# Optimization experiments

Hardware: AMD Instinct MI355X
Metric: run time of the kernel (lower is better)

The kernel has to match this reference:

```python
import jax, jax.numpy as jnp
import numpy as np

B, LT, D, N, H = 16, 512, 1024, 4096, 16
LN_EPS = 1e-5


def setup_inputs() -> dict:
    key = jax.random.key(0)
    ks = jax.random.split(key, 10)
    s = 0.02
    struct_token = jax.random.normal(ks[0], (N, D), dtype=jnp.float32)
    text_token = jax.random.normal(ks[1], (B, LT, D), dtype=jnp.float32)
    # contiguous, sorted segment ids: 256 struct tokens per batch element
    struct_batch = jnp.repeat(jnp.arange(B, dtype=jnp.int32), N // B)
    return {
        "struct_token": struct_token,
        "text_token": text_token,
        "in_proj_w": jax.random.normal(ks[2], (3 * D, D), dtype=jnp.float32) * s,
        "in_proj_b": jnp.zeros((3 * D,), jnp.float32),
        "attn_out_w": jax.random.normal(ks[3], (D, D), dtype=jnp.float32) * s,
        "attn_out_b": jnp.zeros((D,), jnp.float32),
        "ln_g": jnp.ones((D,), jnp.float32),
        "ln_b": jnp.zeros((D,), jnp.float32),
        "proj_w": jax.random.normal(ks[4], (D, D), dtype=jnp.float32) * s,
        "proj_b": jnp.zeros((D,), jnp.float32),
        "struct_batch": struct_batch,
        "L_max": N // B,
    }


def reference(struct_token, text_token, in_proj_w, in_proj_b, attn_out_w,
              attn_out_b, ln_g, ln_b, proj_w, proj_b, struct_batch, L_max):
    Bq = text_token.shape[0]
    Dm = struct_token.shape[-1]
    dh = Dm // H
    Ntok = struct_token.shape[0]

    # ---- ragged pad-pack (struct_batch is sorted/contiguous per segment) ----
    counts = jnp.bincount(struct_batch, length=Bq)                 # [B]
    starts = jnp.concatenate([jnp.zeros((1,), counts.dtype),
                              jnp.cumsum(counts)[:-1]])            # [B]
    pos = jnp.arange(Ntok) - starts[struct_batch]                  # [N] position in segment
    padded = jnp.zeros((Bq, L_max, Dm), struct_token.dtype)
    padded = padded.at[struct_batch, pos].set(struct_token)        # [B, Ls, D]

    # ---- nn.MultiheadAttention (batch_first): Q=padded, K=V=text ----
    wq, wk, wv = in_proj_w[:Dm], in_proj_w[Dm:2 * Dm], in_proj_w[2 * Dm:]
    bq, bk, bv = in_proj_b[:Dm], in_proj_b[Dm:2 * Dm], in_proj_b[2 * Dm:]
    q = (padded @ wq.T + bq).reshape(Bq, L_max, H, dh)
    k = (text_token @ wk.T + bk).reshape(Bq, -1, H, dh)
    v = (text_token @ wv.T + bv).reshape(Bq, -1, H, dh)
    scores = jnp.einsum('bqhd,bkhd->bhqk', q, k) / jnp.sqrt(jnp.float32(dh))
    attn = jax.nn.softmax(scores, axis=-1)
    ctx = jnp.einsum('bhqk,bkhd->bqhd', attn, v).reshape(Bq, L_max, Dm)
    fused = ctx @ attn_out_w.T + attn_out_b                        # [B, Ls, D]

    # ---- LayerNorm + output projection ----
    mu = fused.mean(-1, keepdims=True)
    var = fused.var(-1, keepdims=True)
    fused = (fused - mu) * jax.lax.rsqrt(var + LN_EPS) * ln_g + ln_b
    fused = fused @ proj_w.T + proj_b

    # ---- unpack valid tokens + scatter-mean over segments ----
    tok = fused[struct_batch, pos]                                 # [N, D]
    seg_sum = jax.ops.segment_sum(tok, struct_batch, num_segments=Bq)
    return seg_sum / jnp.maximum(counts, 1)[:, None].astype(seg_sum.dtype)
```

## Files before the change

kernel.cpp:

```cpp
#include <hip/hip_runtime.h>

constexpr int B  = 16;
constexpr int LT = 512;
constexpr int D  = 1024;
constexpr int N  = 4096;
constexpr int H  = 16;
constexpr int DH = D / H;
constexpr int LMAX = N / B;
constexpr float LN_EPS = 1e-5f;

typedef short  s16x8 __attribute__((ext_vector_type(8)));
typedef float  f32x4 __attribute__((ext_vector_type(4)));

__device__ __forceinline__ unsigned short f2bf(float x) {
    unsigned int u = __float_as_uint(x);
    unsigned int r = (u + 0x7fffu + ((u >> 16) & 1u)) >> 16;
    return (unsigned short)r;
}

__device__ __forceinline__ void load_lds16(const void* g, void* l) {
    __builtin_amdgcn_global_load_lds(
        (const __attribute__((address_space(1))) unsigned int*)g,
        (__attribute__((address_space(3))) unsigned int*)l, 16, 0, 0);
}

__global__ void prep_kernel(const int* __restrict__ sb, int* __restrict__ counts,
                            int* __restrict__ starts, int* __restrict__ pos) {
    __shared__ int s_counts[B], s_starts[B];
    int t = threadIdx.x;
    if (t < B) s_counts[t] = 0;
    __syncthreads();
    for (int i = t; i < N; i += 256) atomicAdd(&s_counts[sb[i]], 1);
    __syncthreads();
    if (t == 0) {
        int run = 0;
        for (int b = 0; b < B; b++) { s_starts[b] = run; run += s_counts[b]; }
    }
    __syncthreads();
    if (t < B) { counts[t] = s_counts[t]; starts[t] = s_starts[t]; }
    for (int i = t; i < N; i += 256) {
        int b = sb[i];
        pos[i] = i - s_starts[b];
    }
}

__global__ void scatter_kernel(const float* __restrict__ st, const int* __restrict__ sb,
                               const int* __restrict__ pos, unsigned short* __restrict__ padded) {
    int i = blockIdx.x;
    int b = sb[i], p = pos[i];
    int d = threadIdx.x * 4;
    float4 v = *(const float4*)&st[(size_t)i * D + d];
    ushort4 o;
    o.x = f2bf(v.x); o.y = f2bf(v.y); o.z = f2bf(v.z); o.w = f2bf(v.w);
    *(ushort4*)&padded[((size_t)(b * LMAX + p)) * D + d] = o;
}

__global__ __launch_bounds__(256) void cast3_kernel(
        const float* __restrict__ x0, unsigned short* __restrict__ y0, int n0,
        const float* __restrict__ x1, unsigned short* __restrict__ y1, int n1,
        const float* __restrict__ x2, unsigned short* __restrict__ y2, int n2) {
    long long i = (long long)(blockIdx.x * 256 + threadIdx.x) * 8;
    const float* x; unsigned short* y;
    if (i < n0)                { x = x0 + i; y = y0 + i; }
    else if (i < (long long)n0 + n1) { long long j = i - n0; x = x1 + j; y = y1 + j; }
    else if (i < (long long)n0 + n1 + n2) { long long j = i - n0 - n1; x = x2 + j; y = y2 + j; }
    else return;
    float4 a = *(const float4*)x;
    float4 b = *(const float4*)(x + 4);
    ushort4 o1, o2;
    o1.x = f2bf(a.x); o1.y = f2bf(a.y); o1.z = f2bf(a.z); o1.w = f2bf(a.w);
    o2.x = f2bf(b.x); o2.y = f2bf(b.y); o2.z = f2bf(b.z); o2.w = f2bf(b.w);
    *(ushort4*)y = o1;
    *(ushort4*)(y + 4) = o2;
}

template<typename OutT, bool BIAS_ROW>
__device__ __forceinline__ void gemm_tile(const unsigned short* __restrict__ A,
                                          const unsigned short* __restrict__ W,
                                          const float* __restrict__ bias,
                                          OutT* __restrict__ C,
                                          int Nn, int K, int m0, int n0,
                                          unsigned short* As, unsigned short* Bs) {
    const int tid  = threadIdx.x;
    const int lane = tid & 63;
    const int wave = tid >> 6;
    const int wm = (wave >> 1) * 64, wn = (wave & 1) * 64;

    const int srow = tid >> 2;
    const int scol = (tid & 3) * 8;
    const unsigned short* Ag = A + (size_t)(m0 + srow) * K + scol;
    const unsigned short* Wg = W + (size_t)(n0 + srow) * K + scol;
    unsigned short* Asl = As + tid * 8;
    unsigned short* Bsl = Bs + tid * 8;

    const int fm = lane & 15;
    const int fk = (lane >> 4) * 8;

    f32x4 acc[4][4];
#pragma unroll
    for (int i = 0; i < 4; i++)
#pragma unroll
        for (int j = 0; j < 4; j++) acc[i][j] = (f32x4){0.f, 0.f, 0.f, 0.f};

    for (int k0 = 0; k0 < K; k0 += 32) {
        __syncthreads();
        load_lds16(Ag + k0, Asl);
        load_lds16(Ag + (size_t)64 * K + k0, Asl + 64 * 32);
        load_lds16(Wg + k0, Bsl);
        load_lds16(Wg + (size_t)64 * K + k0, Bsl + 64 * 32);
        __syncthreads();

        s16x8 af[4], bf[4];
#pragma unroll
        for (int i = 0; i < 4; i++) {
            af[i] = *(const s16x8*)&As[(wm + i * 16 + fm) * 32 + fk];
            bf[i] = *(const s16x8*)&Bs[(wn + i * 16 + fm) * 32 + fk];
        }
#pragma unroll
        for (int i = 0; i < 4; i++)
#pragma unroll
            for (int j = 0; j < 4; j++)
                acc[i][j] = __builtin_amdgcn_mfma_f32_16x16x32_bf16(af[i], bf[j], acc[i][j], 0, 0, 0);
    }

    const int fr = (lane >> 4) * 4;
#pragma unroll
    for (int j = 0; j < 4; j++) {
        int col = n0 + wn + j * 16 + fm;
        float bc = BIAS_ROW ? 0.f : bias[col];
#pragma unroll
        for (int i = 0; i < 4; i++) {
            size_t rbase = (size_t)(m0 + wm + i * 16 + fr) * Nn + col;
#pragma unroll
            for (int r = 0; r < 4; r++) {
                float val = acc[i][j][r] + (BIAS_ROW ? bias[m0 + wm + i * 16 + fr + r] : bc);
                if constexpr (sizeof(OutT) == 2)
                    C[rbase + (size_t)r * Nn] = (OutT)f2bf(val);
                else
                    C[rbase + (size_t)r * Nn] = (OutT)val;
            }
        }
    }
}

__global__ __launch_bounds__(256) void qkv_fused(const unsigned short* __restrict__ padded,
                                                 const unsigned short* __restrict__ text,
                                                 const unsigned short* __restrict__ wqkv,
                                                 const float* __restrict__ bqkv,
                                                 unsigned short* __restrict__ qb,
                                                 unsigned short* __restrict__ kb,
                                                 unsigned short* __restrict__ vtb) {
    __shared__ __align__(16) unsigned short As[128 * 32];
    __shared__ __align__(16) unsigned short Bs[128 * 32];
    int flat = blockIdx.x;
    if (flat < 256) {
        gemm_tile<unsigned short, false>(padded, wqkv, bqkv, qb,
                                         D, D, (flat >> 3) * 128, (flat & 7) * 128, As, Bs);
    } else if (flat < 768) {
        int f = flat - 256;
        gemm_tile<unsigned short, false>(text, wqkv + (size_t)D * D, bqkv + D, kb,
                                         D, D, (f >> 3) * 128, (f & 7) * 128, As, Bs);
    } else {
        int f = flat - 768;
        gemm_tile<unsigned short, true>(wqkv + 2 * (size_t)D * D, text, bqkv + 2 * D, vtb,
                                        B * LT, D, (f >> 6) * 128, (f & 63) * 128, As, Bs);
    }
}

__global__ __launch_bounds__(256) void gemm_f32(const unsigned short* __restrict__ A,
                                                const unsigned short* __restrict__ W,
                                                const float* __restrict__ bias,
                                                float* __restrict__ C, int Nn, int K) {
    __shared__ __align__(16) unsigned short As[128 * 32];
    __shared__ __align__(16) unsigned short Bs[128 * 32];
    gemm_tile<float, false>(A, W, bias, C, Nn, K,
                            blockIdx.y * 128, blockIdx.x * 128, As, Bs);
}

__global__ __launch_bounds__(256) void attn_mfma(const unsigned short* __restrict__ qb,
                                                 const unsigned short* __restrict__ kb,
                                                 const unsigned short* __restrict__ vtb,
                                                 unsigned short* __restrict__ ctx) {
    __shared__ __align__(16) unsigned short KV[128 * 72];
    __shared__ __align__(16) unsigned short Ps[4 * 16 * 136];

    const int tid = threadIdx.x;
    const int lane = tid & 63;
    const int wv = tid >> 6;
    const int fm = lane & 15;
    const int quad = lane >> 4;
    const int b = blockIdx.z, h = blockIdx.y;
    const int q0 = blockIdx.x * 64 + wv * 16;

    const size_t qrow = (size_t)(b * LMAX + q0 + fm) * D + h * DH;
    const s16x8 aq0 = *(const s16x8*)&qb[qrow + quad * 8];
    const s16x8 aq1 = *(const s16x8*)&qb[qrow + 32 + quad * 8];

    f32x4 sc[32];
#pragma unroll
    for (int t = 0; t < 32; t++) sc[t] = (f32x4){0.f, 0.f, 0.f, 0.f};

    const size_t kbase = (size_t)(b * LT) * D + h * DH;
    for (int c = 0; c < 4; c++) {
        __syncthreads();
#pragma unroll
        for (int it = 0; it < 4; it++) {
            int e = it * 2048 + tid * 8;
            int row = e >> 6, col = e & 63;
            *(s16x8*)&KV[row * 72 + col] =
                *(const s16x8*)&kb[kbase + (size_t)(c * 128 + row) * D + col];
        }
        __syncthreads();
#pragma unroll
        for (int t = 0; t < 8; t++) {
            s16x8 bk0 = *(const s16x8*)&KV[(t * 16 + fm) * 72 + quad * 8];
            s16x8 bk1 = *(const s16x8*)&KV[(t * 16 + fm) * 72 + 32 + quad * 8];
            f32x4 a = sc[c * 8 + t];
            a = __builtin_amdgcn_mfma_f32_16x16x32_bf16(aq0, bk0, a, 0, 0, 0);
            a = __builtin_amdgcn_mfma_f32_16x16x32_bf16(aq1, bk1, a, 0, 0, 0);
            sc[c * 8 + t] = a;
        }
    }

    const float scale = 0.125f;
    float mx[4], l[4], inv[4];
#pragma unroll
    for (int r = 0; r < 4; r++) {
        float m = sc[0][r];
#pragma unroll
        for (int t = 1; t < 32; t++) m = fmaxf(m, sc[t][r]);
        mx[r] = m;
    }
#pragma unroll
    for (int o = 1; o < 16; o <<= 1)
#pragma unroll
        for (int r = 0; r < 4; r++) mx[r] = fmaxf(mx[r], __shfl_xor(mx[r], o));
#pragma unroll
    for (int r = 0; r < 4; r++) l[r] = 0.f;
#pragma unroll
    for (int t = 0; t < 32; t++)
#pragma unroll
        for (int r = 0; r < 4; r++) {
            float e = __expf((sc[t][r] - mx[r]) * scale);
            sc[t][r] = e;
            l[r] += e;
        }
#pragma unroll
    for (int o = 1; o < 16; o <<= 1)
#pragma unroll
        for (int r = 0; r < 4; r++) l[r] += __shfl_xor(l[r], o);
#pragma unroll
    for (int r = 0; r < 4; r++) inv[r] = 1.f / l[r];

    f32x4 co[4];
#pragma unroll
    for (int n = 0; n < 4; n++) co[n] = (f32x4){0.f, 0.f, 0.f, 0.f};
    unsigned short* Pw = Ps + wv * (16 * 136);
    const size_t vbase = (size_t)(h * DH) * (B * LT) + (size_t)b * LT;

    for (int c = 0; c < 4; c++) {
        __syncthreads();
#pragma unroll
        for (int it = 0; it < 4; it++) {
            int e = it * 2048 + tid * 8;
            int row = e >> 7, col = e & 127;
            *(s16x8*)&KV[row * 136 + col] =
                *(const s16x8*)&vtb[vbase + (size_t)row * (B * LT) + c * 128 + col];
        }
#pragma unroll
        for (int t = 0; t < 8; t++)
#pragma unroll
            for (int r = 0; r < 4; r++)
                Pw[(quad * 4 + r) * 136 + t * 16 + fm] = f2bf(sc[c * 8 + t][r]);
        __syncthreads();
#pragma unroll
        for (int s = 0; s < 4; s++) {
            s16x8 ap = *(const s16x8*)&Pw[fm * 136 + s * 32 + quad * 8];
#pragma unroll
            for (int n = 0; n < 4; n++) {
                s16x8 bv = *(const s16x8*)&KV[(n * 16 + fm) * 136 + s * 32 + quad * 8];
                co[n] = __builtin_amdgcn_mfma_f32_16x16x32_bf16(ap, bv, co[n], 0, 0, 0);
            }
        }
    }

    const size_t obase = (size_t)(b * LMAX + q0) * D + h * DH;
#pragma unroll
    for (int n = 0; n < 4; n++)
#pragma unroll
        for (int r = 0; r < 4; r++)
            ctx[obase + (size_t)(quad * 4 + r) * D + n * 16 + fm] = f2bf(co[n][r] * inv[r]);
}

__global__ __launch_bounds__(256) void lnmean_kernel(const float* __restrict__ f1,
                                                     const float* __restrict__ g,
                                                     const float* __restrict__ bb,
                                                     const int* __restrict__ counts,
                                                     float* __restrict__ msum) {
    int b = blockIdx.x;
    int cnt = counts[b];
    int s0 = blockIdx.y * 32;
    int s1 = min(cnt, s0 + 32);
    if (s0 >= s1) return;
    int t = threadIdx.x;
    int wv = t >> 6, ln = t & 63;
    float4 gg = ((const float4*)g)[t];
    float4 bv = ((const float4*)bb)[t];
    float acc[4] = {0.f, 0.f, 0.f, 0.f};
    __shared__ float red[8];

    for (int s = s0; s < s1; s++) {
        const float* x = f1 + ((size_t)(b * LMAX + s)) * D;
        float4 val = ((const float4*)x)[t];
        float sm = val.x + val.y + val.z + val.w;
        float ss = val.x * val.x + val.y * val.y + val.z * val.z + val.w * val.w;
#pragma unroll
        for (int o = 32; o; o >>= 1) { sm += __shfl_xor(sm, o); ss += __shfl_xor(ss, o); }
        if (ln == 0) { red[wv] = sm; red[4 + wv] = ss; }
        __syncthreads();
        sm = red[0] + red[1] + red[2] + red[3];
        ss = red[4] + red[5] + red[6] + red[7];
        __syncthreads();
        float mu = sm * (1.f / D);
        float var = ss * (1.f / D) - mu * mu;
        float r = rsqrtf(var + LN_EPS);
        acc[0] += (val.x - mu) * r * gg.x + bv.x;
        acc[1] += (val.y - mu) * r * gg.y + bv.y;
        acc[2] += (val.z - mu) * r * gg.z + bv.z;
        acc[3] += (val.w - mu) * r * gg.w + bv.w;
    }
    float inv = 1.f / (float)max(cnt, 1);
#pragma unroll
    for (int j = 0; j < 4; j++)
        atomicAdd(&msum[(size_t)b * D + t * 4 + j], acc[j] * inv);
}

__global__ __launch_bounds__(256) void tproj_kernel(const float* __restrict__ msum,
                                                    const float* __restrict__ W,
                                                    const float* __restrict__ bias,
                                                    float* __restrict__ out) {
    int lane = threadIdx.x & 63;
    int n = blockIdx.x * 4 + (threadIdx.x >> 6);
    float4 wr[4];
#pragma unroll
    for (int i = 0; i < 4; i++)
        wr[i] = *(const float4*)&W[(size_t)n * D + i * 256 + lane * 4];
    float bn = bias[n];
    for (int b = 0; b < B; b++) {
        float s = 0.f;
#pragma unroll
        for (int i = 0; i < 4; i++) {
            float4 m4 = *(const float4*)&msum[(size_t)b * D + i * 256 + lane * 4];
            s += m4.x * wr[i].x + m4.y * wr[i].y + m4.z * wr[i].z + m4.w * wr[i].w;
        }
#pragma unroll
        for (int o = 32; o; o >>= 1) s += __shfl_xor(s, o);
        if (lane == 0) out[(size_t)b * D + n] = s + bn;
    }
}

extern "C" void kernel_launch(void* const* d_in, const int* in_sizes, int n_in,
                              void* d_out, int out_size, void* d_ws, size_t ws_size,
                              hipStream_t stream) {
    const float* struct_token = (const float*)d_in[0];
    const float* text_token   = (const float*)d_in[1];
    const float* in_proj_w    = (const float*)d_in[2];
    const float* in_proj_b    = (const float*)d_in[3];
    const float* attn_out_w   = (const float*)d_in[4];
    const float* attn_out_b   = (const float*)d_in[5];
    const float* ln_g         = (const float*)d_in[6];
    const float* ln_b         = (const float*)d_in[7];
    const float* proj_w       = (const float*)d_in[8];
    const float* proj_b       = (const float*)d_in[9];
    const int*   sb           = (const int*)d_in[10];
    float* out = (float*)d_out;

    const size_t MQ  = (size_t)B * LMAX;
    const size_t MKV = (size_t)B * LT;

    char* p = (char*)d_ws;
    unsigned short* padded_b = (unsigned short*)p;  p += MQ * D * 2;
    unsigned short* text_b   = (unsigned short*)p;  p += MKV * D * 2;
    unsigned short* wqkv_b   = (unsigned short*)p;  p += (size_t)3 * D * D * 2;
    unsigned short* wattn_b  = (unsigned short*)p;  p += (size_t)D * D * 2;
    unsigned short* qb       = (unsigned short*)p;  p += MQ * D * 2;
    unsigned short* kb       = (unsigned short*)p;  p += MKV * D * 2;
    unsigned short* vtb      = (unsigned short*)p;  p += MKV * D * 2;
    unsigned short* ctx_b    = (unsigned short*)p;  p += MQ * D * 2;
    float* f1   = (float*)p;  p += MQ * D * 4;
    float* msum = (float*)p;  p += (size_t)B * D * 4;
    int* pos    = (int*)p;  p += N * 4;
    int* counts = (int*)p;  p += B * 4;
    int* starts = (int*)p;  p += B * 4;

    hipMemsetAsync(padded_b, 0, MQ * D * 2, stream);
    hipMemsetAsync(msum, 0, (size_t)B * D * 4, stream);
    prep_kernel<<<1, 256, 0, stream>>>(sb, counts, starts, pos);
    scatter_kernel<<<N, 256, 0, stream>>>(struct_token, sb, pos, padded_b);

    cast3_kernel<<<6144, 256, 0, stream>>>(
        text_token, text_b, (int)(MKV * D),
        in_proj_w,  wqkv_b, 3 * D * D,
        attn_out_w, wattn_b, D * D);

    qkv_fused<<<1280, 256, 0, stream>>>(padded_b, text_b, wqkv_b, in_proj_b, qb, kb, vtb);

    attn_mfma<<<dim3(LMAX / 64, H, B), 256, 0, stream>>>(qb, kb, vtb, ctx_b);

    gemm_f32<<<dim3(D / 128, MQ / 128), 256, 0, stream>>>(ctx_b, wattn_b, attn_out_b, f1, D, D);

    lnmean_kernel<<<dim3(B, LMAX / 32), 256, 0, stream>>>(f1, ln_g, ln_b, counts, msum);

    tproj_kernel<<<256, 256, 0, stream>>>(msum, proj_w, proj_b, out);
}
```

Baseline: 306.8 us.

## Double GEMM K-step, read K/V straight from global in attention, store attn-out as bf16

The GEMM tile now loads two 32-wide K panels per barrier pair, halving the number of synchronisations per K loop. The attention kernel drops its LDS staging of K and V^T and reads MFMA operands directly from global memory. The attention output projection now writes bf16 instead of fp32, and the LayerNorm/mean kernel reads bf16, halving that intermediate's traffic. The trade-offs are bf16 rounding before LayerNorm, double the GEMM LDS footprint, and possibly uncoalesced global reads in attention.

Result: slower. 345.1 us (+12.5%).

```diff
diff --git a/kernel.cpp b/kernel.cpp
--- a/kernel.cpp
+++ b/kernel.cpp
@@ -16,6 +16,9 @@
     unsigned int u = __float_as_uint(x);
     unsigned int r = (u + 0x7fffu + ((u >> 16) & 1u)) >> 16;
     return (unsigned short)r;
+}
+__device__ __forceinline__ float bf2f(unsigned short u) {
+    return __uint_as_float((unsigned int)u << 16);
 }
 
 __device__ __forceinline__ void load_lds16(const void* g, void* l) {
@@ -74,6 +77,8 @@
     *(ushort4*)(y + 4) = o2;
 }
 
+constexpr int PANEL = 128 * 32;
+
 template<typename OutT, bool BIAS_ROW>
 __device__ __forceinline__ void gemm_tile(const unsigned short* __restrict__ A,
                                           const unsigned short* __restrict__ W,
@@ -102,25 +107,34 @@
 #pragma unroll
         for (int j = 0; j < 4; j++) acc[i][j] = (f32x4){0.f, 0.f, 0.f, 0.f};
 
-    for (int k0 = 0; k0 < K; k0 += 32) {
+    for (int k0 = 0; k0 < K; k0 += 64) {
         __syncthreads();
         load_lds16(Ag + k0, Asl);
         load_lds16(Ag + (size_t)64 * K + k0, Asl + 64 * 32);
         load_lds16(Wg + k0, Bsl);
         load_lds16(Wg + (size_t)64 * K + k0, Bsl + 64 * 32);
-        __syncthreads();
-
-        s16x8 af[4], bf[4];
-#pragma unroll
-        for (int i = 0; i < 4; i++) {
-            af[i] = *(const s16x8*)&As[(wm + i * 16 + fm) * 32 + fk];
-            bf[i] = *(const s16x8*)&Bs[(wn + i * 16 + fm) * 32 + fk];
+        load_lds16(Ag + k0 + 32, Asl + PANEL);
+        load_lds16(Ag + (size_t)64 * K + k0 + 32, Asl + PANEL + 64 * 32);
+        load_lds16(Wg + k0 + 32, Bsl + PANEL);
+        load_lds16(Wg + (size_t)64 * K + k0 + 32, Bsl + PANEL + 64 * 32);
+        __syncthreads();
+
+#pragma unroll
+        for (int hp = 0; hp < 2; hp++) {
+            const unsigned short* Ap = As + hp * PANEL;
+            const unsigned short* Bp = Bs + hp * PANEL;
+            s16x8 af[4], bf[4];
+#pragma unroll
+            for (int i = 0; i < 4; i++) {
+                af[i] = *(const s16x8*)&Ap[(wm + i * 16 + fm) * 32 + fk];
+                bf[i] = *(const s16x8*)&Bp[(wn + i * 16 + fm) * 32 + fk];
+            }
+#pragma unroll
+            for (int i = 0; i < 4; i++)
+#pragma unroll
+                for (int j = 0; j < 4; j++)
+                    acc[i][j] = __builtin_amdgcn_mfma_f32_16x16x32_bf16(af[i], bf[j], acc[i][j], 0, 0, 0);
         }
-#pragma unroll
-        for (int i = 0; i < 4; i++)
-#pragma unroll
-            for (int j = 0; j < 4; j++)
-                acc[i][j] = __builtin_amdgcn_mfma_f32_16x16x32_bf16(af[i], bf[j], acc[i][j], 0, 0, 0);
     }
 
     const int fr = (lane >> 4) * 4;
@@ -150,8 +164,8 @@
                                                  unsigned short* __restrict__ qb,
                                                  unsigned short* __restrict__ kb,
                                                  unsigned short* __restrict__ vtb) {
-    __shared__ __align__(16) unsigned short As[128 * 32];
-    __shared__ __align__(16) unsigned short Bs[128 * 32];
+    __shared__ __align__(16) unsigned short As[2 * PANEL];
+    __shared__ __align__(16) unsigned short Bs[2 * PANEL];
     int flat = blockIdx.x;
     if (flat < 256) {
         gemm_tile<unsigned short, false>(padded, wqkv, bqkv, qb,
@@ -167,21 +181,20 @@
     }
 }
 
-__global__ __launch_bounds__(256) void gemm_f32(const unsigned short* __restrict__ A,
-                                                const unsigned short* __restrict__ W,
-                                                const float* __restrict__ bias,
-                                                float* __restrict__ C, int Nn, int K) {
-    __shared__ __align__(16) unsigned short As[128 * 32];
-    __shared__ __align__(16) unsigned short Bs[128 * 32];
-    gemm_tile<float, false>(A, W, bias, C, Nn, K,
-                            blockIdx.y * 128, blockIdx.x * 128, As, Bs);
+__global__ __launch_bounds__(256) void gemm_bf(const unsigned short* __restrict__ A,
+                                               const unsigned short* __restrict__ W,
+                                               const float* __restrict__ bias,
+                                               unsigned short* __restrict__ C, int Nn, int K) {
+    __shared__ __align__(16) unsigned short As[2 * PANEL];
+    __shared__ __align__(16) unsigned short Bs[2 * PANEL];
+    gemm_tile<unsigned short, false>(A, W, bias, C, Nn, K,
+                                     blockIdx.y * 128, blockIdx.x * 128, As, Bs);
 }
 
 __global__ __launch_bounds__(256) void attn_mfma(const unsigned short* __restrict__ qb,
                                                  const unsigned short* __restrict__ kb,
                                                  const unsigned short* __restrict__ vtb,
                                                  unsigned short* __restrict__ ctx) {
-    __shared__ __align__(16) unsigned short KV[128 * 72];
     __shared__ __align__(16) unsigned short Ps[4 * 16 * 136];
 
     const int tid = threadIdx.x;
@@ -197,29 +210,16 @@
     const s16x8 aq1 = *(const s16x8*)&qb[qrow + 32 + quad * 8];
 
     f32x4 sc[32];
-#pragma unroll
-    for (int t = 0; t < 32; t++) sc[t] = (f32x4){0.f, 0.f, 0.f, 0.f};
-
-    const size_t kbase = (size_t)(b * LT) * D + h * DH;
-    for (int c = 0; c < 4; c++) {
-        __syncthreads();
-#pragma unroll
-        for (int it = 0; it < 4; it++) {
-            int e = it * 2048 + tid * 8;
-            int row = e >> 6, col = e & 63;
-            *(s16x8*)&KV[row * 72 + col] =
-                *(const s16x8*)&kb[kbase + (size_t)(c * 128 + row) * D + col];
-        }
-        __syncthreads();
-#pragma unroll
-        for (int t = 0; t < 8; t++) {
-            s16x8 bk0 = *(const s16x8*)&KV[(t * 16 + fm) * 72 + quad * 8];
-            s16x8 bk1 = *(const s16x8*)&KV[(t * 16 + fm) * 72 + 32 + quad * 8];
-            f32x4 a = sc[c * 8 + t];
-            a = __builtin_amdgcn_mfma_f32_16x16x32_bf16(aq0, bk0, a, 0, 0, 0);
-            a = __builtin_amdgcn_mfma_f32_16x16x32_bf16(aq1, bk1, a, 0, 0, 0);
-            sc[c * 8 + t] = a;
-        }
+    const unsigned short* kr = kb + (size_t)(b * LT) * D + h * DH + (size_t)fm * D + quad * 8;
+#pragma unroll
+    for (int t = 0; t < 32; t++) {
+        s16x8 bk0 = *(const s16x8*)kr;
+        s16x8 bk1 = *(const s16x8*)(kr + 32);
+        f32x4 a = (f32x4){0.f, 0.f, 0.f, 0.f};
+        a = __builtin_amdgcn_mfma_f32_16x16x32_bf16(aq0, bk0, a, 0, 0, 0);
+        a = __builtin_amdgcn_mfma_f32_16x16x32_bf16(aq1, bk1, a, 0, 0, 0);
+        sc[t] = a;
+        kr += 16 * D;
     }
 
     const float scale = 0.125f;
@@ -256,17 +256,10 @@
 #pragma unroll
     for (int n = 0; n < 4; n++) co[n] = (f32x4){0.f, 0.f, 0.f, 0.f};
     unsigned short* Pw = Ps + wv * (16 * 136);
-    const size_t vbase = (size_t)(h * DH) * (B * LT) + (size_t)b * LT;
+    const unsigned short* vr0 = vtb + (size_t)(h * DH) * (B * LT) + (size_t)b * LT
+                                    + (size_t)fm * (B * LT) + quad * 8;
 
     for (int c = 0; c < 4; c++) {
-        __syncthreads();
-#pragma unroll
-        for (int it = 0; it < 4; it++) {
-            int e = it * 2048 + tid * 8;
-            int row = e >> 7, col = e & 127;
-            *(s16x8*)&KV[row * 136 + col] =
-                *(const s16x8*)&vtb[vbase + (size_t)row * (B * LT) + c * 128 + col];
-        }
 #pragma unroll
         for (int t = 0; t < 8; t++)
 #pragma unroll
@@ -278,10 +271,11 @@
             s16x8 ap = *(const s16x8*)&Pw[fm * 136 + s * 32 + quad * 8];
 #pragma unroll
             for (int n = 0; n < 4; n++) {
-                s16x8 bv = *(const s16x8*)&KV[(n * 16 + fm) * 136 + s * 32 + quad * 8];
+                s16x8 bv = *(const s16x8*)(vr0 + (size_t)(n * 16) * (B * LT) + c * 128 + s * 32);
                 co[n] = __builtin_amdgcn_mfma_f32_16x16x32_bf16(ap, bv, co[n], 0, 0, 0);
             }
         }
+        __syncthreads();
     }
 
     const size_t obase = (size_t)(b * LMAX + q0) * D + h * DH;
@@ -292,7 +286,7 @@
             ctx[obase + (size_t)(quad * 4 + r) * D + n * 16 + fm] = f2bf(co[n][r] * inv[r]);
 }
 
-__global__ __launch_bounds__(256) void lnmean_kernel(const float* __restrict__ f1,
+__global__ __launch_bounds__(256) void lnmean_kernel(const unsigned short* __restrict__ f1,
                                                      const float* __restrict__ g,
                                                      const float* __restrict__ bb,
                                                      const int* __restrict__ counts,
@@ -310,8 +304,9 @@
     __shared__ float red[8];
 
     for (int s = s0; s < s1; s++) {
-        const float* x = f1 + ((size_t)(b * LMAX + s)) * D;
-        float4 val = ((const float4*)x)[t];
+        const unsigned short* x = f1 + ((size_t)(b * LMAX + s)) * D;
+        ushort4 u = ((const ushort4*)x)[t];
+        float4 val = {bf2f(u.x), bf2f(u.y), bf2f(u.z), bf2f(u.w)};
         float sm = val.x + val.y + val.z + val.w;
         float ss = val.x * val.x + val.y * val.y + val.z * val.z + val.w * val.w;
 #pragma unroll
@@ -387,7 +382,7 @@
     unsigned short* kb       = (unsigned short*)p;  p += MKV * D * 2;
     unsigned short* vtb      = (unsigned short*)p;  p += MKV * D * 2;
     unsigned short* ctx_b    = (unsigned short*)p;  p += MQ * D * 2;
-    float* f1   = (float*)p;  p += MQ * D * 4;
+    unsigned short* f1b      = (unsigned short*)p;  p += MQ * D * 2;
     float* msum = (float*)p;  p += (size_t)B * D * 4;
     int* pos    = (int*)p;  p += N * 4;
     int* counts = (int*)p;  p += B * 4;
@@ -407,9 +402,9 @@
 
     attn_mfma<<<dim3(LMAX / 64, H, B), 256, 0, stream>>>(qb, kb, vtb, ctx_b);
 
-    gemm_f32<<<dim3(D / 128, MQ / 128), 256, 0, stream>>>(ctx_b, wattn_b, attn_out_b, f1, D, D);
-
-    lnmean_kernel<<<dim3(B, LMAX / 32), 256, 0, stream>>>(f1, ln_g, ln_b, counts, msum);
+    gemm_bf<<<dim3(D / 128, MQ / 128), 256, 0, stream>>>(ctx_b, wattn_b, attn_out_b, f1b, D, D);
+
+    lnmean_kernel<<<dim3(B, LMAX / 32), 256, 0, stream>>>(f1b, ln_g, ln_b, counts, msum);
 
     tproj_kernel<<<256, 256, 0, stream>>>(msum, proj_w, proj_b, out);
 }
```
